# Kernel tuning notes

Hardware: AMD Instinct MI355X
Metric: run time of the kernel (lower is better)

The kernel has to match this reference:

```python
import jax, jax.numpy as jnp
import numpy as np

N = 50000      # nodes
E = 800000     # edges (avg degree 16)
IN = 128       # input_dim
HID = 64       # hidden_dim
HEADS = 2      # heads in layer 1
OUT = 32       # output_dim
NEG_SLOPE = 0.2


def setup_inputs() -> dict:
    key = jax.random.key(0)
    ks = jax.random.split(key, 8)
    s = 0.1
    x = jax.random.normal(ks[0], (N, IN), jnp.float32)
    edge_index = jax.random.randint(ks[1], (2, E), 0, N, dtype=jnp.int64)
    W1 = jax.random.normal(ks[2], (IN, HEADS * HID), jnp.float32) * s
    att_src1 = jax.random.normal(ks[3], (HEADS, HID), jnp.float32) * s
    att_dst1 = jax.random.normal(ks[4], (HEADS, HID), jnp.float32) * s
    bias1 = jnp.zeros((HEADS * HID,), jnp.float32)
    W2 = jax.random.normal(ks[5], (HEADS * HID, OUT), jnp.float32) * s
    att_src2 = jax.random.normal(ks[6], (1, OUT), jnp.float32) * s
    att_dst2 = jax.random.normal(ks[7], (1, OUT), jnp.float32) * s
    bias2 = jnp.zeros((OUT,), jnp.float32)
    return {"x": x, "edge_index": edge_index,
            "W1": W1, "att_src1": att_src1, "att_dst1": att_dst1, "bias1": bias1,
            "W2": W2, "att_src2": att_src2, "att_dst2": att_dst2, "bias2": bias2}


def gat_conv(x, src, dst, W, a_src, a_dst, bias, heads, out_ch, concat):
    # PyG GATConv: linear -> per-node attn terms -> per-edge LeakyReLU score
    # -> segment softmax over incoming edges of each dst -> weighted scatter-sum.
    n = x.shape[0]
    h = (x @ W).reshape(n, heads, out_ch)                 # [N,H,C]
    a_s = jnp.einsum('nhc,hc->nh', h, a_src)              # [N,H]
    a_d = jnp.einsum('nhc,hc->nh', h, a_dst)              # [N,H]
    e = jax.nn.leaky_relu(a_s[src] + a_d[dst], NEG_SLOPE) # [E,H]
    e_max = jax.ops.segment_max(e, dst, num_segments=n)   # [N,H] (self-loops => no empty segment)
    ex = jnp.exp(e - e_max[dst])
    denom = jax.ops.segment_sum(ex, dst, num_segments=n)
    alpha = ex / denom[dst]                               # [E,H]
    msg = h[src] * alpha[..., None]                       # [E,H,C]
    out = jax.ops.segment_sum(msg, dst, num_segments=n)   # [N,H,C]
    out = out.reshape(n, heads * out_ch) if concat else out.mean(axis=1)
    return out + bias


def reference(x, edge_index, W1, att_src1, att_dst1, bias1, W2, att_src2, att_dst2, bias2):
    # add self-loops (PyG default add_self_loops=True)
    loops = jnp.arange(N, dtype=edge_index.dtype)
    src = jnp.concatenate([edge_index[0], loops])
    dst = jnp.concatenate([edge_index[1], loops])
    h = gat_conv(x, src, dst, W1, att_src1, att_dst1, bias1, HEADS, HID, True)
    h = jax.nn.elu(h)
    out = gat_conv(h, src, dst, W2, att_src2, att_dst2, bias2, 1, OUT, False)
    return out
```

## Files before the change

### kernel.cpp

```cpp
#include <hip/hip_runtime.h>
#include <hip/hip_bf16.h>
#include <math.h>

#define NN 50000
#define EE 800000
#define NEG 0.2f
#define BKT 64
#define G1_BLKS 782
#define FILL_BLKS 782
#define G2_BLKS 391

#define OFF_H1B    0UL
#define OFF_H2IN   (OFF_H1B + (size_t)NN*128*2)
#define OFF_H2B    (OFF_H2IN + (size_t)NN*128*4)
#define OFF_ASAD1  (OFF_H2B + (size_t)NN*32*2)
#define OFF_ASAD2  (OFF_ASAD1 + (size_t)NN*4*4)
#define OFF_CUR    (OFF_ASAD2 + (size_t)NN*2*4)
#define OFF_BKT    (OFF_CUR + (size_t)NN*4)
#define OFF_FLAG   (OFF_BKT + (size_t)NN*BKT*2 + 256)

__device__ __forceinline__ unsigned short f2bf(float f) {
    unsigned u = __float_as_uint(f);
    unsigned r = (u + 0x7fffu + ((u >> 16) & 1u)) >> 16;
    return (unsigned short)r;
}
__device__ __forceinline__ float bflo(unsigned v) { return __uint_as_float(v << 16); }
__device__ __forceinline__ float bfhi(unsigned v) { return __uint_as_float(v & 0xffff0000u); }

__global__ void k_detect(const int* __restrict__ p, int* __restrict__ flag) {
    int t = threadIdx.x;
    int v = p[2*t + 1];
    unsigned long long b = __ballot(v != 0);
    if (t == 0) flag[0] = (b == 0ULL) ? 1 : 0;
}

__global__ __launch_bounds__(256) void k_build_gemm1(
        const int* __restrict__ raw, const int* __restrict__ flag,
        int* __restrict__ cur, unsigned short* __restrict__ bkt,
        const float* __restrict__ x, const float* __restrict__ W,
        const float* __restrict__ atts, const float* __restrict__ attd,
        unsigned short* __restrict__ h1b, float* __restrict__ asad) {
    __shared__ float Wl[32*128];
    __shared__ float xs[32*76];
    int t = threadIdx.x;

    if (blockIdx.x >= G1_BLKS) {
        int bid = blockIdx.x - G1_BLKS;
        int f = flag[0];
        int base = bid*1024 + t;
        int s[4], d[4]; bool act[4];
        #pragma unroll
        for (int u = 0; u < 4; ++u) {
            int i = base + 256*u;
            act[u] = i < EE;
            int ii = act[u] ? i : 0;
            if (f) { s[u] = raw[2*ii]; d[u] = raw[2*(EE + ii)]; }
            else   { s[u] = raw[ii];   d[u] = raw[EE + ii]; }
        }
        #pragma unroll
        for (int u = 0; u < 4; ++u) {
            if (act[u]) {
                int pos = atomicAdd(&cur[d[u]], 1);
                if (pos < BKT) bkt[(size_t)d[u]*BKT + pos] = (unsigned short)s[u];
            }
        }
        return;
    }

    int bid = blockIdx.x;
    int cg = t & 31, ng = t >> 5;
    int j0 = cg * 4;
    int nb = bid * 64;
    const float4* W4 = (const float4*)W;
    const float4* x4 = (const float4*)x;

    float4 a0={0,0,0,0},a1={0,0,0,0},a2={0,0,0,0},a3={0,0,0,0};
    float4 a4={0,0,0,0},a5={0,0,0,0},a6={0,0,0,0},a7={0,0,0,0};

    for (int k0 = 0; k0 < 128; k0 += 32) {
        __syncthreads();
        #pragma unroll
        for (int i = t; i < 1024; i += 256) {
            int kk = i >> 5, c4 = i & 31;
            *(float4*)&Wl[kk*128 + c4*4] = W4[(size_t)(k0+kk)*32 + c4];
        }
        #pragma unroll
        for (int i = t; i < 512; i += 256) {
            int row = i >> 3, c4 = i & 7;
            float4 v = make_float4(0.f,0.f,0.f,0.f);
            int n = nb + row;
            if (n < NN) v = x4[(size_t)n*32 + (k0>>2) + c4];
            xs[(c4*4+0)*76 + row] = v.x;
            xs[(c4*4+1)*76 + row] = v.y;
            xs[(c4*4+2)*76 + row] = v.z;
            xs[(c4*4+3)*76 + row] = v.w;
        }
        __syncthreads();
        #pragma unroll
        for (int kk = 0; kk < 32; ++kk) {
            float4 w = *(const float4*)&Wl[kk*128 + j0];
            float4 xa = *(const float4*)&xs[kk*76 + ng*8];
            float4 xb = *(const float4*)&xs[kk*76 + ng*8 + 4];
            a0.x += xa.x*w.x; a0.y += xa.x*w.y; a0.z += xa.x*w.z; a0.w += xa.x*w.w;
            a1.x += xa.y*w.x; a1.y += xa.y*w.y; a1.z += xa.y*w.z; a1.w += xa.y*w.w;
            a2.x += xa.z*w.x; a2.y += xa.z*w.y; a2.z += xa.z*w.z; a2.w += xa.z*w.w;
            a3.x += xa.w*w.x; a3.y += xa.w*w.y; a3.z += xa.w*w.z; a3.w += xa.w*w.w;
            a4.x += xb.x*w.x; a4.y += xb.x*w.y; a4.z += xb.x*w.z; a4.w += xb.x*w.w;
            a5.x += xb.y*w.x; a5.y += xb.y*w.y; a5.z += xb.y*w.z; a5.w += xb.y*w.w;
            a6.x += xb.z*w.x; a6.y += xb.z*w.y; a6.z += xb.z*w.z; a6.w += xb.z*w.w;
            a7.x += xb.w*w.x; a7.y += xb.w*w.y; a7.z += xb.w*w.z; a7.w += xb.w*w.w;
        }
    }
    int head = cg >> 4;
    int cb = (cg & 15) * 4;
    float4 s4 = *(const float4*)&atts[head*64 + cb];
    float4 d4 = *(const float4*)&attd[head*64 + cb];
    #define EPI(ai, m) { \
        int n = nb + ng*8 + m; \
        if (n < NN) { \
            ushort4 pk; pk.x = f2bf(ai.x); pk.y = f2bf(ai.y); pk.z = f2bf(ai.z); pk.w = f2bf(ai.w); \
            *(ushort4*)&h1b[(size_t)n*128 + j0] = pk; \
            float ps = ai.x*s4.x + ai.y*s4.y + ai.z*s4.z + ai.w*s4.w; \
            float pd = ai.x*d4.x + ai.y*d4.y + ai.z*d4.z + ai.w*d4.w; \
            ps += __shfl_xor(ps, 1, 64); pd += __shfl_xor(pd, 1, 64); \
            ps += __shfl_xor(ps, 2, 64); pd += __shfl_xor(pd, 2, 64); \
            ps += __shfl_xor(ps, 4, 64); pd += __shfl_xor(pd, 4, 64); \
            ps += __shfl_xor(ps, 8, 64); pd += __shfl_xor(pd, 8, 64); \
            if ((cg & 15) == 0) { asad[(size_t)n*4 + head] = ps; asad[(size_t)n*4 + 2 + head] = pd; } \
        } }
    EPI(a0,0) EPI(a1,1) EPI(a2,2) EPI(a3,3) EPI(a4,4) EPI(a5,5) EPI(a6,6) EPI(a7,7)
    #undef EPI
}

__global__ __launch_bounds__(256) void k_agg1(const uint4* __restrict__ h1q, const float* __restrict__ asad,
                       const int* __restrict__ cur, const unsigned short* __restrict__ bkt,
                       const float* __restrict__ bias, float* __restrict__ h2in) {
    int lane = threadIdx.x & 63;
    int n = blockIdx.x*4 + (threadIdx.x >> 6);
    n = __builtin_amdgcn_readfirstlane(n);
    int cnt = cur[n]; cnt = cnt < BKT ? cnt : BKT;
    int tot = cnt + 1;
    int q = lane >> 4, c = lane & 15;
    float ad0 = asad[(size_t)n*4 + 2], ad1 = asad[(size_t)n*4 + 3];
    bool head1 = c >= 8;
    const unsigned short* row = bkt + (size_t)n*BKT;
    float den = 0.f;
    float a0=0.f,a1=0.f,a2=0.f,a3=0.f,a4=0.f,a5=0.f,a6=0.f,a7=0.f;
    for (int i = 0; i < tot; i += 8) {
        int iA = i + q, iB = i + 4 + q;
        int rA = (int)row[iA & 63], rB = (int)row[iB & 63];
        int sA = (iA < cnt) ? rA : n;
        int sB = (iB < cnt) ? rB : n;
        bool actA = iA < tot, actB = iB < tot;
        float2 asA = *(const float2*)&asad[(size_t)sA*4];
        float2 asB = *(const float2*)&asad[(size_t)sB*4];
        uint4 pvA = h1q[(size_t)sA*16 + c];
        uint4 pvB = h1q[(size_t)sB*16 + c];
        float eA0 = asA.x + ad0; eA0 = (eA0 > 0.f) ? eA0 : NEG*eA0;
        float eA1 = asA.y + ad1; eA1 = (eA1 > 0.f) ? eA1 : NEG*eA1;
        float eB0 = asB.x + ad0; eB0 = (eB0 > 0.f) ? eB0 : NEG*eB0;
        float eB1 = asB.y + ad1; eB1 = (eB1 > 0.f) ? eB1 : NEG*eB1;
        float exA = __expf(head1 ? eA1 : eA0); if (!actA) exA = 0.f;
        float exB = __expf(head1 ? eB1 : eB0); if (!actB) exB = 0.f;
        den += exA + exB;
        a0 += exA*bflo(pvA.x) + exB*bflo(pvB.x);
        a1 += exA*bfhi(pvA.x) + exB*bfhi(pvB.x);
        a2 += exA*bflo(pvA.y) + exB*bflo(pvB.y);
        a3 += exA*bfhi(pvA.y) + exB*bfhi(pvB.y);
        a4 += exA*bflo(pvA.z) + exB*bflo(pvB.z);
        a5 += exA*bfhi(pvA.z) + exB*bfhi(pvB.z);
        a6 += exA*bflo(pvA.w) + exB*bflo(pvB.w);
        a7 += exA*bfhi(pvA.w) + exB*bfhi(pvB.w);
    }
    #define RED(v) v += __shfl_xor(v, 16, 64); v += __shfl_xor(v, 32, 64);
    RED(den) RED(a0) RED(a1) RED(a2) RED(a3) RED(a4) RED(a5) RED(a6) RED(a7)
    #undef RED
    if (q == 0) {
        float4 b0 = *(const float4*)&bias[c*8];
        float4 b1 = *(const float4*)&bias[c*8 + 4];
        float r = 1.f / den;
        float o0 = a0*r + b0.x, o1 = a1*r + b0.y, o2 = a2*r + b0.z, o3 = a3*r + b0.w;
        float o4 = a4*r + b1.x, o5 = a5*r + b1.y, o6 = a6*r + b1.z, o7 = a7*r + b1.w;
        o0 = (o0 > 0.f) ? o0 : expm1f(o0); o1 = (o1 > 0.f) ? o1 : expm1f(o1);
        o2 = (o2 > 0.f) ? o2 : expm1f(o2); o3 = (o3 > 0.f) ? o3 : expm1f(o3);
        o4 = (o4 > 0.f) ? o4 : expm1f(o4); o5 = (o5 > 0.f) ? o5 : expm1f(o5);
        o6 = (o6 > 0.f) ? o6 : expm1f(o6); o7 = (o7 > 0.f) ? o7 : expm1f(o7);
        float4 w0 = {o0,o1,o2,o3}, w1 = {o4,o5,o6,o7};
        *(float4*)&h2in[(size_t)n*128 + c*8] = w0;
        *(float4*)&h2in[(size_t)n*128 + c*8 + 4] = w1;
    }
}

__global__ __launch_bounds__(256) void k_gemm2(const float* __restrict__ xin, const float* __restrict__ W,
                        const float* __restrict__ atts, const float* __restrict__ attd,
                        unsigned short* __restrict__ h2b, float* __restrict__ asad2) {
    __shared__ float Wl[128*32];
    __shared__ float xs[32*132];
    int t = threadIdx.x;
    int cg = t & 7, ng = t >> 3;
    int j0 = cg * 4;
    int nb = blockIdx.x * 128;
    const float4* W4 = (const float4*)W;
    const float4* x4 = (const float4*)xin;
    for (int i = t; i < 1024; i += 256) ((float4*)Wl)[i] = W4[i];

    float4 a0={0,0,0,0},a1={0,0,0,0},a2={0,0,0,0},a3={0,0,0,0};
    for (int k0 = 0; k0 < 128; k0 += 32) {
        __syncthreads();
        #pragma unroll
        for (int i = t; i < 1024; i += 256) {
            int row = i >> 3, c4 = i & 7;
            float4 v = make_float4(0.f,0.f,0.f,0.f);
            int n = nb + row;
            if (n < NN) v = x4[(size_t)n*32 + (k0>>2) + c4];
            xs[(c4*4+0)*132 + row] = v.x;
            xs[(c4*4+1)*132 + row] = v.y;
            xs[(c4*4+2)*132 + row] = v.z;
            xs[(c4*4+3)*132 + row] = v.w;
        }
        __syncthreads();
        #pragma unroll
        for (int kk = 0; kk < 32; ++kk) {
            float4 w = *(const float4*)&Wl[(k0+kk)*32 + j0];
            float4 xa = *(const float4*)&xs[kk*132 + ng*4];
            a0.x += xa.x*w.x; a0.y += xa.x*w.y; a0.z += xa.x*w.z; a0.w += xa.x*w.w;
            a1.x += xa.y*w.x; a1.y += xa.y*w.y; a1.z += xa.y*w.z; a1.w += xa.y*w.w;
            a2.x += xa.z*w.x; a2.y += xa.z*w.y; a2.z += xa.z*w.z; a2.w += xa.z*w.w;
            a3.x += xa.w*w.x; a3.y += xa.w*w.y; a3.z += xa.w*w.z; a3.w += xa.w*w.w;
        }
    }
    float4 s4 = *(const float4*)&atts[j0];
    float4 d4 = *(const float4*)&attd[j0];
    #define EPI(ai, m) { \
        int n = nb + ng*4 + m; \
        if (n < NN) { \
            ushort4 pk; pk.x = f2bf(ai.x); pk.y = f2bf(ai.y); pk.z = f2bf(ai.z); pk.w = f2bf(ai.w); \
            *(ushort4*)&h2b[(size_t)n*32 + j0] = pk; \
            float ps = ai.x*s4.x + ai.y*s4.y + ai.z*s4.z + ai.w*s4.w; \
            float pd = ai.x*d4.x + ai.y*d4.y + ai.z*d4.z + ai.w*d4.w; \
            ps += __shfl_xor(ps, 1, 64); pd += __shfl_xor(pd, 1, 64); \
            ps += __shfl_xor(ps, 2, 64); pd += __shfl_xor(pd, 2, 64); \
            ps += __shfl_xor(ps, 4, 64); pd += __shfl_xor(pd, 4, 64); \
            if (cg == 0) { asad2[(size_t)n*2] = ps; asad2[(size_t)n*2 + 1] = pd; } \
        } }
    EPI(a0,0) EPI(a1,1) EPI(a2,2) EPI(a3,3)
    #undef EPI
}

__global__ __launch_bounds__(256) void k_agg2(const unsigned* __restrict__ h2u, const float* __restrict__ asad2,
                       const int* __restrict__ cur, const unsigned short* __restrict__ bkt,
                       const float* __restrict__ bias, float* __restrict__ out) {
    int lane = threadIdx.x & 63;
    int n = blockIdx.x*4 + (threadIdx.x >> 6);
    n = __builtin_amdgcn_readfirstlane(n);
    int cnt = cur[n]; cnt = cnt < BKT ? cnt : BKT;
    int tot = cnt + 1;
    int q = lane >> 4, c = lane & 15;
    float ad = asad2[(size_t)n*2 + 1];
    const unsigned short* row = bkt + (size_t)n*BKT;
    float den = 0.f, aA = 0.f, aB = 0.f;
    for (int i = 0; i < tot; i += 8) {
        int iA = i + q, iB = i + 4 + q;
        int rA = (int)row[iA & 63], rB = (int)row[iB & 63];
        int sA = (iA < cnt) ? rA : n;
        int sB = (iB < cnt) ? rB : n;
        bool actA = iA < tot, actB = iB < tot;
        float eA = asad2[(size_t)sA*2] + ad; eA = (eA > 0.f) ? eA : NEG*eA;
        float eB = asad2[(size_t)sB*2] + ad; eB = (eB > 0.f) ? eB : NEG*eB;
        unsigned pA = h2u[(size_t)sA*16 + c];
        unsigned pB = h2u[(size_t)sB*16 + c];
        float exA = __expf(eA); if (!actA) exA = 0.f;
        float exB = __expf(eB); if (!actB) exB = 0.f;
        den += exA + exB;
        aA += exA*bflo(pA) + exB*bflo(pB);
        aB += exA*bfhi(pA) + exB*bfhi(pB);
    }
    #define RED(v) v += __shfl_xor(v, 16, 64); v += __shfl_xor(v, 32, 64);
    RED(den) RED(aA) RED(aB)
    #undef RED
    if (q == 0) {
        float2 bb = ((const float2*)bias)[c];
        float r = 1.f / den;
        float2 ov; ov.x = aA*r + bb.x; ov.y = aB*r + bb.y;
        ((float2*)out)[(size_t)n*16 + c] = ov;
    }
}

extern "C" void kernel_launch(void* const* d_in, const int* in_sizes, int n_in,
                              void* d_out, int out_size, void* d_ws, size_t ws_size,
                              hipStream_t stream) {
    (void)in_sizes; (void)n_in; (void)out_size; (void)ws_size;
    const float* x   = (const float*)d_in[0];
    const int*   er  = (const int*)d_in[1];
    const float* W1  = (const float*)d_in[2];
    const float* as1 = (const float*)d_in[3];
    const float* ad1 = (const float*)d_in[4];
    const float* b1  = (const float*)d_in[5];
    const float* W2  = (const float*)d_in[6];
    const float* as2 = (const float*)d_in[7];
    const float* ad2 = (const float*)d_in[8];
    const float* b2  = (const float*)d_in[9];
    float* out = (float*)d_out;
    char* ws = (char*)d_ws;

    unsigned short* h1b = (unsigned short*)(ws + OFF_H1B);
    float* h2in  = (float*)(ws + OFF_H2IN);
    unsigned short* h2b = (unsigned short*)(ws + OFF_H2B);
    float* asad1 = (float*)(ws + OFF_ASAD1);
    float* asd2  = (float*)(ws + OFF_ASAD2);
    int*   cur   = (int*)(ws + OFF_CUR);
    unsigned short* bkt = (unsigned short*)(ws + OFF_BKT);
    int*   flag  = (int*)(ws + OFF_FLAG);

    hipMemsetAsync(ws + OFF_CUR, 0, (size_t)NN*4, stream);
    k_detect<<<1, 64, 0, stream>>>(er, flag);
    k_build_gemm1<<<G1_BLKS + FILL_BLKS, 256, 0, stream>>>(er, flag, cur, bkt,
                                                           x, W1, as1, ad1, h1b, asad1);
    k_agg1<<<NN/4, 256, 0, stream>>>((const uint4*)h1b, asad1, cur, bkt, b1, h2in);
    k_gemm2<<<G2_BLKS, 256, 0, stream>>>(h2in, W2, as2, ad2, h2b, asd2);
    k_agg2<<<NN/4, 256, 0, stream>>>((const unsigned*)h2b, asd2, cur, bkt, b2, out);
}
```

Baseline: 214.6 us.

## Fuse layer-2 GEMM into layer-1 aggregation and widen gather unroll

Folds the layer-2 linear projection and its attention-term computation into the layer-1 aggregation kernel. The ELU-activated row stays in shared memory and is multiplied by W2, which is staged in LDS by each block. This removes the 25.6MB fp32 h2in write/read round trip and one kernel launch. Each 4-node block now reloads the 16KB W2 into LDS and adds a __syncthreads. Separately, both aggregation loops now gather 4 neighbours per lane per iteration instead of 2, to increase memory-level parallelism.

```diff
diff --git a/kernel.cpp b/kernel.cpp
--- a/kernel.cpp
+++ b/kernel.cpp
@@ -8,11 +8,9 @@
 #define BKT 64
 #define G1_BLKS 782
 #define FILL_BLKS 782
-#define G2_BLKS 391
 
 #define OFF_H1B    0UL
-#define OFF_H2IN   (OFF_H1B + (size_t)NN*128*2)
-#define OFF_H2B    (OFF_H2IN + (size_t)NN*128*4)
+#define OFF_H2B    (OFF_H1B + (size_t)NN*128*2)
 #define OFF_ASAD1  (OFF_H2B + (size_t)NN*32*2)
 #define OFF_ASAD2  (OFF_ASAD1 + (size_t)NN*4*4)
 #define OFF_CUR    (OFF_ASAD2 + (size_t)NN*2*4)
@@ -132,11 +130,19 @@
     #undef EPI
 }
 
-__global__ __launch_bounds__(256) void k_agg1(const uint4* __restrict__ h1q, const float* __restrict__ asad,
+__global__ __launch_bounds__(256) void k_agg1f(const uint4* __restrict__ h1q, const float* __restrict__ asad,
                        const int* __restrict__ cur, const unsigned short* __restrict__ bkt,
-                       const float* __restrict__ bias, float* __restrict__ h2in) {
-    int lane = threadIdx.x & 63;
-    int n = blockIdx.x*4 + (threadIdx.x >> 6);
+                       const float* __restrict__ bias,
+                       const float* __restrict__ atts2, const float* __restrict__ attd2,
+                       const float* __restrict__ W2,
+                       unsigned short* __restrict__ h2b, float* __restrict__ asad2) {
+    __shared__ float W2l[128*32];
+    __shared__ float hrow[4][128];
+    int t = threadIdx.x;
+    int lane = t & 63, wid = t >> 6;
+    for (int i = t; i < 1024; i += 256) ((float4*)W2l)[i] = ((const float4*)W2)[i];
+
+    int n = blockIdx.x*4 + wid;
     n = __builtin_amdgcn_readfirstlane(n);
     int cnt = cur[n]; cnt = cnt < BKT ? cnt : BKT;
     int tot = cnt + 1;
@@ -146,105 +152,90 @@
     const unsigned short* row = bkt + (size_t)n*BKT;
     float den = 0.f;
     float a0=0.f,a1=0.f,a2=0.f,a3=0.f,a4=0.f,a5=0.f,a6=0.f,a7=0.f;
-    for (int i = 0; i < tot; i += 8) {
-        int iA = i + q, iB = i + 4 + q;
-        int rA = (int)row[iA & 63], rB = (int)row[iB & 63];
-        int sA = (iA < cnt) ? rA : n;
-        int sB = (iB < cnt) ? rB : n;
-        bool actA = iA < tot, actB = iB < tot;
-        float2 asA = *(const float2*)&asad[(size_t)sA*4];
-        float2 asB = *(const float2*)&asad[(size_t)sB*4];
-        uint4 pvA = h1q[(size_t)sA*16 + c];
-        uint4 pvB = h1q[(size_t)sB*16 + c];
-        float eA0 = asA.x + ad0; eA0 = (eA0 > 0.f) ? eA0 : NEG*eA0;
-        float eA1 = asA.y + ad1; eA1 = (eA1 > 0.f) ? eA1 : NEG*eA1;
-        float eB0 = asB.x + ad0; eB0 = (eB0 > 0.f) ? eB0 : NEG*eB0;
-        float eB1 = asB.y + ad1; eB1 = (eB1 > 0.f) ? eB1 : NEG*eB1;
-        float exA = __expf(head1 ? eA1 : eA0); if (!actA) exA = 0.f;
-        float exB = __expf(head1 ? eB1 : eB0); if (!actB) exB = 0.f;
-        den += exA + exB;
-        a0 += exA*bflo(pvA.x) + exB*bflo(pvB.x);
-        a1 += exA*bfhi(pvA.x) + exB*bfhi(pvB.x);
-        a2 += exA*bflo(pvA.y) + exB*bflo(pvB.y);
-        a3 += exA*bfhi(pvA.y) + exB*bfhi(pvB.y);
-        a4 += exA*bflo(pvA.z) + exB*bflo(pvB.z);
-        a5 += exA*bfhi(pvA.z) + exB*bfhi(pvB.z);
-        a6 += exA*bflo(pvA.w) + exB*bflo(pvB.w);
-        a7 += exA*bfhi(pvA.w) + exB*bfhi(pvB.w);
+    for (int i = 0; i < tot; i += 16) {
+        int i0 = i+q, i1 = i+4+q, i2 = i+8+q, i3 = i+12+q;
+        int r0 = (int)row[i0 & 63], r1 = (int)row[i1 & 63];
+        int r2 = (int)row[i2 & 63], r3 = (int)row[i3 & 63];
+        int s0 = (i0 < cnt) ? r0 : n, s1 = (i1 < cnt) ? r1 : n;
+        int s2 = (i2 < cnt) ? r2 : n, s3 = (i3 < cnt) ? r3 : n;
+        bool ac0 = i0 < tot, ac1 = i1 < tot, ac2 = i2 < tot, ac3 = i3 < tot;
+        float2 w0 = *(const float2*)&asad[(size_t)s0*4];
+        float2 w1 = *(const float2*)&asad[(size_t)s1*4];
+        float2 w2 = *(const float2*)&asad[(size_t)s2*4];
+        float2 w3 = *(const float2*)&asad[(size_t)s3*4];
+        uint4 p0 = h1q[(size_t)s0*16 + c];
+        uint4 p1 = h1q[(size_t)s1*16 + c];
+        uint4 p2 = h1q[(size_t)s2*16 + c];
+        uint4 p3 = h1q[(size_t)s3*16 + c];
+        #define SCORE(wv, ac) ({ \
+            float e0 = wv.x + ad0; e0 = (e0 > 0.f) ? e0 : NEG*e0; \
+            float e1 = wv.y + ad1; e1 = (e1 > 0.f) ? e1 : NEG*e1; \
+            float ex = __expf(head1 ? e1 : e0); if (!(ac)) ex = 0.f; ex; })
+        float x0 = SCORE(w0, ac0), x1 = SCORE(w1, ac1);
+        float x2 = SCORE(w2, ac2), x3 = SCORE(w3, ac3);
+        #undef SCORE
+        den += (x0 + x1) + (x2 + x3);
+        a0 += x0*bflo(p0.x) + x1*bflo(p1.x) + x2*bflo(p2.x) + x3*bflo(p3.x);
+        a1 += x0*bfhi(p0.x) + x1*bfhi(p1.x) + x2*bfhi(p2.x) + x3*bfhi(p3.x);
+        a2 += x0*bflo(p0.y) + x1*bflo(p1.y) + x2*bflo(p2.y) + x3*bflo(p3.y);
+        a3 += x0*bfhi(p0.y) + x1*bfhi(p1.y) + x2*bfhi(p2.y) + x3*bfhi(p3.y);
+        a4 += x0*bflo(p0.z) + x1*bflo(p1.z) + x2*bflo(p2.z) + x3*bflo(p3.z);
+        a5 += x0*bfhi(p0.z) + x1*bfhi(p1.z) + x2*bfhi(p2.z) + x3*bfhi(p3.z);
+        a6 += x0*bflo(p0.w) + x1*bflo(p1.w) + x2*bflo(p2.w) + x3*bflo(p3.w);
+        a7 += x0*bfhi(p0.w) + x1*bfhi(p1.w) + x2*bfhi(p2.w) + x3*bfhi(p3.w);
     }
     #define RED(v) v += __shfl_xor(v, 16, 64); v += __shfl_xor(v, 32, 64);
     RED(den) RED(a0) RED(a1) RED(a2) RED(a3) RED(a4) RED(a5) RED(a6) RED(a7)
     #undef RED
-    if (q == 0) {
+    {
         float4 b0 = *(const float4*)&bias[c*8];
         float4 b1 = *(const float4*)&bias[c*8 + 4];
         float r = 1.f / den;
-        float o0 = a0*r + b0.x, o1 = a1*r + b0.y, o2 = a2*r + b0.z, o3 = a3*r + b0.w;
-        float o4 = a4*r + b1.x, o5 = a5*r + b1.y, o6 = a6*r + b1.z, o7 = a7*r + b1.w;
-        o0 = (o0 > 0.f) ? o0 : expm1f(o0); o1 = (o1 > 0.f) ? o1 : expm1f(o1);
-        o2 = (o2 > 0.f) ? o2 : expm1f(o2); o3 = (o3 > 0.f) ? o3 : expm1f(o3);
-        o4 = (o4 > 0.f) ? o4 : expm1f(o4); o5 = (o5 > 0.f) ? o5 : expm1f(o5);
-        o6 = (o6 > 0.f) ? o6 : expm1f(o6); o7 = (o7 > 0.f) ? o7 : expm1f(o7);
-        float4 w0 = {o0,o1,o2,o3}, w1 = {o4,o5,o6,o7};
-        *(float4*)&h2in[(size_t)n*128 + c*8] = w0;
-        *(float4*)&h2in[(size_t)n*128 + c*8 + 4] = w1;
-    }
-}
-
-__global__ __launch_bounds__(256) void k_gemm2(const float* __restrict__ xin, const float* __restrict__ W,
-                        const float* __restrict__ atts, const float* __restrict__ attd,
-                        unsigned short* __restrict__ h2b, float* __restrict__ asad2) {
-    __shared__ float Wl[128*32];
-    __shared__ float xs[32*132];
-    int t = threadIdx.x;
-    int cg = t & 7, ng = t >> 3;
-    int j0 = cg * 4;
-    int nb = blockIdx.x * 128;
-    const float4* W4 = (const float4*)W;
-    const float4* x4 = (const float4*)xin;
-    for (int i = t; i < 1024; i += 256) ((float4*)Wl)[i] = W4[i];
-
-    float4 a0={0,0,0,0},a1={0,0,0,0},a2={0,0,0,0},a3={0,0,0,0};
-    for (int k0 = 0; k0 < 128; k0 += 32) {
-        __syncthreads();
-        #pragma unroll
-        for (int i = t; i < 1024; i += 256) {
-            int row = i >> 3, c4 = i & 7;
-            float4 v = make_float4(0.f,0.f,0.f,0.f);
-            int n = nb + row;
-            if (n < NN) v = x4[(size_t)n*32 + (k0>>2) + c4];
-            xs[(c4*4+0)*132 + row] = v.x;
-            xs[(c4*4+1)*132 + row] = v.y;
-            xs[(c4*4+2)*132 + row] = v.z;
-            xs[(c4*4+3)*132 + row] = v.w;
-        }
-        __syncthreads();
-        #pragma unroll
-        for (int kk = 0; kk < 32; ++kk) {
-            float4 w = *(const float4*)&Wl[(k0+kk)*32 + j0];
-            float4 xa = *(const float4*)&xs[kk*132 + ng*4];
-            a0.x += xa.x*w.x; a0.y += xa.x*w.y; a0.z += xa.x*w.z; a0.w += xa.x*w.w;
-            a1.x += xa.y*w.x; a1.y += xa.y*w.y; a1.z += xa.y*w.z; a1.w += xa.y*w.w;
-            a2.x += xa.z*w.x; a2.y += xa.z*w.y; a2.z += xa.z*w.z; a2.w += xa.z*w.w;
-            a3.x += xa.w*w.x; a3.y += xa.w*w.y; a3.z += xa.w*w.z; a3.w += xa.w*w.w;
-        }
-    }
-    float4 s4 = *(const float4*)&atts[j0];
-    float4 d4 = *(const float4*)&attd[j0];
-    #define EPI(ai, m) { \
-        int n = nb + ng*4 + m; \
-        if (n < NN) { \
-            ushort4 pk; pk.x = f2bf(ai.x); pk.y = f2bf(ai.y); pk.z = f2bf(ai.z); pk.w = f2bf(ai.w); \
-            *(ushort4*)&h2b[(size_t)n*32 + j0] = pk; \
-            float ps = ai.x*s4.x + ai.y*s4.y + ai.z*s4.z + ai.w*s4.w; \
-            float pd = ai.x*d4.x + ai.y*d4.y + ai.z*d4.z + ai.w*d4.w; \
-            ps += __shfl_xor(ps, 1, 64); pd += __shfl_xor(pd, 1, 64); \
-            ps += __shfl_xor(ps, 2, 64); pd += __shfl_xor(pd, 2, 64); \
-            ps += __shfl_xor(ps, 4, 64); pd += __shfl_xor(pd, 4, 64); \
-            if (cg == 0) { asad2[(size_t)n*2] = ps; asad2[(size_t)n*2 + 1] = pd; } \
-        } }
-    EPI(a0,0) EPI(a1,1) EPI(a2,2) EPI(a3,3)
-    #undef EPI
+        a0 = a0*r + b0.x; a1 = a1*r + b0.y; a2 = a2*r + b0.z; a3 = a3*r + b0.w;
+        a4 = a4*r + b1.x; a5 = a5*r + b1.y; a6 = a6*r + b1.z; a7 = a7*r + b1.w;
+        a0 = (a0 > 0.f) ? a0 : expm1f(a0); a1 = (a1 > 0.f) ? a1 : expm1f(a1);
+        a2 = (a2 > 0.f) ? a2 : expm1f(a2); a3 = (a3 > 0.f) ? a3 : expm1f(a3);
+        a4 = (a4 > 0.f) ? a4 : expm1f(a4); a5 = (a5 > 0.f) ? a5 : expm1f(a5);
+        a6 = (a6 > 0.f) ? a6 : expm1f(a6); a7 = (a7 > 0.f) ? a7 : expm1f(a7);
+        if (q == 0) {
+            float4 v0 = {a0,a1,a2,a3}, v1 = {a4,a5,a6,a7};
+            *(float4*)&hrow[wid][c*8] = v0;
+            *(float4*)&hrow[wid][c*8 + 4] = v1;
+        }
+    }
+    __syncthreads();
+    {
+        int j = lane & 31;
+        int kbase = (lane >> 5) * 64;
+        float acc0 = 0.f, acc1 = 0.f, acc2 = 0.f, acc3 = 0.f;
+        const float* hr = hrow[wid];
+        #pragma unroll
+        for (int k4 = 0; k4 < 16; k4 += 4) {
+            float4 h0 = *(const float4*)&hr[kbase + k4*4];
+            float4 h1v = *(const float4*)&hr[kbase + k4*4 + 4];
+            float4 h2v = *(const float4*)&hr[kbase + k4*4 + 8];
+            float4 h3v = *(const float4*)&hr[kbase + k4*4 + 12];
+            acc0 += h0.x*W2l[(kbase+k4*4+0)*32+j]  + h0.y*W2l[(kbase+k4*4+1)*32+j]
+                  + h0.z*W2l[(kbase+k4*4+2)*32+j]  + h0.w*W2l[(kbase+k4*4+3)*32+j];
+            acc1 += h1v.x*W2l[(kbase+k4*4+4)*32+j] + h1v.y*W2l[(kbase+k4*4+5)*32+j]
+                  + h1v.z*W2l[(kbase+k4*4+6)*32+j] + h1v.w*W2l[(kbase+k4*4+7)*32+j];
+            acc2 += h2v.x*W2l[(kbase+k4*4+8)*32+j] + h2v.y*W2l[(kbase+k4*4+9)*32+j]
+                  + h2v.z*W2l[(kbase+k4*4+10)*32+j]+ h2v.w*W2l[(kbase+k4*4+11)*32+j];
+            acc3 += h3v.x*W2l[(kbase+k4*4+12)*32+j]+ h3v.y*W2l[(kbase+k4*4+13)*32+j]
+                  + h3v.z*W2l[(kbase+k4*4+14)*32+j]+ h3v.w*W2l[(kbase+k4*4+15)*32+j];
+        }
+        float acc = (acc0 + acc1) + (acc2 + acc3);
+        acc += __shfl_xor(acc, 32, 64);
+        float ps = acc * atts2[j];
+        float pd = acc * attd2[j];
+        ps += __shfl_xor(ps, 1, 64); pd += __shfl_xor(pd, 1, 64);
+        ps += __shfl_xor(ps, 2, 64); pd += __shfl_xor(pd, 2, 64);
+        ps += __shfl_xor(ps, 4, 64); pd += __shfl_xor(pd, 4, 64);
+        ps += __shfl_xor(ps, 8, 64); pd += __shfl_xor(pd, 8, 64);
+        ps += __shfl_xor(ps, 16, 64); pd += __shfl_xor(pd, 16, 64);
+        if (lane < 32) h2b[(size_t)n*32 + j] = f2bf(acc);
+        if (lane == 0) { asad2[(size_t)n*2] = ps; asad2[(size_t)n*2 + 1] = pd; }
+    }
 }
 
 __global__ __launch_bounds__(256) void k_agg2(const unsigned* __restrict__ h2u, const float* __restrict__ asad2,
@@ -259,21 +250,28 @@
     float ad = asad2[(size_t)n*2 + 1];
     const unsigned short* row = bkt + (size_t)n*BKT;
     float den = 0.f, aA = 0.f, aB = 0.f;
-    for (int i = 0; i < tot; i += 8) {
-        int iA = i + q, iB = i + 4 + q;
-        int rA = (int)row[iA & 63], rB = (int)row[iB & 63];
-        int sA = (iA < cnt) ? rA : n;
-        int sB = (iB < cnt) ? rB : n;
-        bool actA = iA < tot, actB = iB < tot;
-        float eA = asad2[(size_t)sA*2] + ad; eA = (eA > 0.f) ? eA : NEG*eA;
-        float eB = asad2[(size_t)sB*2] + ad; eB = (eB > 0.f) ? eB : NEG*eB;
-        unsigned pA = h2u[(size_t)sA*16 + c];
-        unsigned pB = h2u[(size_t)sB*16 + c];
-        float exA = __expf(eA); if (!actA) exA = 0.f;
-        float exB = __expf(eB); if (!actB) exB = 0.f;
-        den += exA + exB;
-        aA += exA*bflo(pA) + exB*bflo(pB);
-        aB += exA*bfhi(pA) + exB*bfhi(pB);
+    for (int i = 0; i < tot; i += 16) {
+        int i0 = i+q, i1 = i+4+q, i2 = i+8+q, i3 = i+12+q;
+        int r0 = (int)row[i0 & 63], r1 = (int)row[i1 & 63];
+        int r2 = (int)row[i2 & 63], r3 = (int)row[i3 & 63];
+        int s0 = (i0 < cnt) ? r0 : n, s1 = (i1 < cnt) ? r1 : n;
+        int s2 = (i2 < cnt) ? r2 : n, s3 = (i3 < cnt) ? r3 : n;
+        bool ac0 = i0 < tot, ac1 = i1 < tot, ac2 = i2 < tot, ac3 = i3 < tot;
+        float e0 = asad2[(size_t)s0*2] + ad; e0 = (e0 > 0.f) ? e0 : NEG*e0;
+        float e1 = asad2[(size_t)s1*2] + ad; e1 = (e1 > 0.f) ? e1 : NEG*e1;
+        float e2 = asad2[(size_t)s2*2] + ad; e2 = (e2 > 0.f) ? e2 : NEG*e2;
+        float e3 = asad2[(size_t)s3*2] + ad; e3 = (e3 > 0.f) ? e3 : NEG*e3;
+        unsigned p0 = h2u[(size_t)s0*16 + c];
+        unsigned p1 = h2u[(size_t)s1*16 + c];
+        unsigned p2 = h2u[(size_t)s2*16 + c];
+        unsigned p3 = h2u[(size_t)s3*16 + c];
+        float x0 = __expf(e0); if (!ac0) x0 = 0.f;
+        float x1 = __expf(e1); if (!ac1) x1 = 0.f;
+        float x2 = __expf(e2); if (!ac2) x2 = 0.f;
+        float x3 = __expf(e3); if (!ac3) x3 = 0.f;
+        den += (x0 + x1) + (x2 + x3);
+        aA += x0*bflo(p0) + x1*bflo(p1) + x2*bflo(p2) + x3*bflo(p3);
+        aB += x0*bfhi(p0) + x1*bfhi(p1) + x2*bfhi(p2) + x3*bfhi(p3);
     }
     #define RED(v) v += __shfl_xor(v, 16, 64); v += __shfl_xor(v, 32, 64);
     RED(den) RED(aA) RED(aB)
@@ -304,7 +302,6 @@
     char* ws = (char*)d_ws;
 
     unsigned short* h1b = (unsigned short*)(ws + OFF_H1B);
-    float* h2in  = (float*)(ws + OFF_H2IN);
     unsigned short* h2b = (unsigned short*)(ws + OFF_H2B);
     float* asad1 = (float*)(ws + OFF_ASAD1);
     float* asd2  = (float*)(ws + OFF_ASAD2);
@@ -316,7 +313,7 @@
     k_detect<<<1, 64, 0, stream>>>(er, flag);
     k_build_gemm1<<<G1_BLKS + FILL_BLKS, 256, 0, stream>>>(er, flag, cur, bkt,
                                                            x, W1, as1, ad1, h1b, asad1);
-    k_agg1<<<NN/4, 256, 0, stream>>>((const uint4*)h1b, asad1, cur, bkt, b1, h2in);
-    k_gemm2<<<G2_BLKS, 256, 0, stream>>>(h2in, W2, as2, ad2, h2b, asd2);
+    k_agg1f<<<NN/4, 256, 0, stream>>>((const uint4*)h1b, asad1, cur, bkt, b1,
+                                      as2, ad2, W2, h2b, asd2);
     k_agg2<<<NN/4, 256, 0, stream>>>((const unsigned*)h2b, asd2, cur, bkt, b2, out);
 }
```

Result: slower. 223.8 us (+4.3%).
